# Kernel tuning notes

Hardware: AMD Instinct MI355X
Metric: run time of the kernel (lower is better)

## Reference

```python
import jax, jax.numpy as jnp
import numpy as np

N_EMBD = 1024
EXPAND = 2
D_INNER = N_EMBD * EXPAND          # 2048
D_STATE = 64
N_HEADS = D_INNER // D_STATE       # 32
HEAD_DIM = D_INNER // N_HEADS      # 64
N_GROUPS = 1
D_CONV = 4
N_LAYERS = 48
BATCH, SEQ = 1, 512
PROJ_SIZE = 2 * D_INNER + N_HEADS + 2 * N_GROUPS * D_STATE  # 4256
EPS = 1e-6


def setup_inputs() -> dict:
    key = jax.random.key(0)
    ks = jax.random.split(key, 6)
    init_std = 0.02
    proj_std = 0.02 / np.sqrt(2 * N_LAYERS)
    return {
        "x": jax.random.normal(ks[0], (BATCH, SEQ, N_EMBD), jnp.float32),
        "norm_scale": jnp.ones((N_EMBD,), jnp.float32),
        "w_in": jax.random.normal(ks[1], (N_EMBD, PROJ_SIZE), jnp.float32) * init_std,
        "conv_weight": jax.random.normal(ks[2], (D_CONV, D_INNER), jnp.float32) * 0.02,
        "conv_bias": jnp.zeros((D_INNER,), jnp.float32),
        "A_log": jnp.log(0.5 + jnp.arange(N_HEADS, dtype=jnp.float32) * 0.5 / N_HEADS),
        "dt_bias": jax.random.normal(ks[3], (N_HEADS,), jnp.float32) * 0.1,
        "w_out": jax.random.normal(ks[4], (D_INNER, N_EMBD), jnp.float32) * proj_std,
    }


def _mamba_fwd(x, norm_scale, w_in, conv_weight, conv_bias, A_log, dt_bias, w_out):
    b, T, _ = x.shape
    residual = x
    # RMSNorm
    xn = x * jax.lax.rsqrt(jnp.mean(x * x, axis=-1, keepdims=True) + EPS) * norm_scale
    # in_proj and split
    proj = xn @ w_in  # (b, T, proj_size)
    gate = proj[..., :D_INNER]
    ssm_in = proj[..., D_INNER:2 * D_INNER]
    dt_raw = proj[..., 2 * D_INNER:2 * D_INNER + N_HEADS]
    gs = N_GROUPS * D_STATE
    B = proj[..., 2 * D_INNER + N_HEADS:2 * D_INNER + N_HEADS + gs].reshape(b, T, N_GROUPS, D_STATE)
    C = proj[..., 2 * D_INNER + N_HEADS + gs:].reshape(b, T, N_GROUPS, D_STATE)
    # causal depthwise short conv (cross-correlation, matching lax.conv semantics)
    xp = jnp.pad(ssm_in, ((0, 0), (D_CONV - 1, 0), (0, 0)))
    conv = conv_bias + sum(conv_weight[k] * xp[:, k:k + T, :] for k in range(D_CONV))
    h = jax.nn.silu(conv)  # (b, T, d_inner)
    dt = jax.nn.softplus(dt_raw + dt_bias)  # (b, T, H)
    A = -jnp.exp(A_log)  # (H,)
    A_bar = jnp.exp(A[None, None, :] * dt)  # (b, T, H)
    # heads / groups
    hpg = N_HEADS // N_GROUPS
    xh = h.reshape(b, T, N_HEADS, HEAD_DIM)
    Bh = jnp.repeat(B, hpg, axis=2)  # (b, T, H, N)
    Ch = jnp.repeat(C, hpg, axis=2)  # (b, T, H, N)
    # Bu[b,t,h,p,n] = B[b,t,h,n] * dt[b,t,h] * x[b,t,h,p]
    Bu = Bh[:, :, :, None, :] * (dt[..., None, None] * xh[..., None])  # (b,T,H,P,N)

    def _binary_op(left, right):
        a_l, b_l = left
        a_r, b_r = right
        return (a_l * a_r, a_r * b_l + b_r)

    # A_bar broadcast to (b,T,H,1,1) so the pair broadcasts against Bu
    _, states = jax.lax.associative_scan(_binary_op, (A_bar[..., None, None], Bu), axis=1)
    y = jnp.einsum('bthpn,bthn->bthp', states, Ch).reshape(b, T, D_INNER)
    y = y * jax.nn.silu(gate)
    y = y @ w_out
    return residual + y


def reference(x, norm_scale, w_in, conv_weight, conv_bias, A_log, dt_bias, w_out):
    return _mamba_fwd(x, norm_scale, w_in, conv_weight, conv_bias, A_log, dt_bias, w_out)
```

## Files before the change

### kernel.cpp

```cpp
#include <hip/hip_runtime.h>
#include <hip/hip_bf16.h>

typedef unsigned short u16;
typedef float f32x4v __attribute__((ext_vector_type(4)));
typedef short short8 __attribute__((ext_vector_type(8)));

#define TSEQ 512
#define EMB  1024
#define DI   2048
#define NH   32
#define DS   64
#define PROJ 4256
#define PROJP 4352
#define NCH  8
#define LCH  64
#define KSPLIT2 4

#define MFMA16(a, b, c) __builtin_amdgcn_mfma_f32_16x16x32_bf16(a, b, c, 0, 0, 0)

__device__ __forceinline__ u16 f2bf(float f) {
    union { __hip_bfloat16 h; u16 u; } cv;
    cv.h = __float2bfloat16(f);
    return cv.u;
}
__device__ __forceinline__ unsigned pack2(float a, float b) {
    return (unsigned)f2bf(a) | ((unsigned)f2bf(b) << 16);
}
__device__ __forceinline__ float silu(float v) { return v / (1.f + expf(-v)); }

__device__ __forceinline__ void transpose_tile(
        const float* __restrict__ src, u16* __restrict__ dst,
        int K, int N, int n0, int k0, int tid, float tile[64][68]) {
    const int lr = tid >> 4;
    const int lc = tid & 15;
    #pragma unroll
    for (int ps = 0; ps < 4; ++ps) {
        int r = ps * 16 + lr;
        float4 v;
        if (n0 + lc * 4 + 3 < N) {
            v = *(const float4*)&src[(size_t)(k0 + r) * N + n0 + lc * 4];
        } else {
            float t0 = 0.f, t1 = 0.f, t2 = 0.f, t3 = 0.f;
            int nb = n0 + lc * 4;
            if (nb + 0 < N) t0 = src[(size_t)(k0 + r) * N + nb + 0];
            if (nb + 1 < N) t1 = src[(size_t)(k0 + r) * N + nb + 1];
            if (nb + 2 < N) t2 = src[(size_t)(k0 + r) * N + nb + 2];
            if (nb + 3 < N) t3 = src[(size_t)(k0 + r) * N + nb + 3];
            v = make_float4(t0, t1, t2, t3);
        }
        *(float4*)&tile[r][lc * 4] = v;
    }
    __syncthreads();
    const int kk2 = (tid & 31) * 2;
    const int nr  = tid >> 5;
    #pragma unroll
    for (int ps = 0; ps < 8; ++ps) {
        int n = ps * 8 + nr;
        unsigned o = (unsigned)f2bf(tile[kk2][n]) | ((unsigned)f2bf(tile[kk2 + 1][n]) << 16);
        *(unsigned*)&dst[(size_t)(n0 + n) * K + k0 + kk2] = o;
    }
}

__global__ __launch_bounds__(256) void k_prep(
        const float* __restrict__ w_in, u16* __restrict__ w_inT,
        const float* __restrict__ w_out, u16* __restrict__ w_outT,
        const float* __restrict__ x, const float* __restrict__ scale,
        u16* __restrict__ xnb) {
    __shared__ float tile[64][68];
    const int b = blockIdx.x;
    const int tid = threadIdx.x;
    if (b < 1088) {
        int bx = b % 68, by = b / 68;
        transpose_tile(w_in, w_inT, 1024, PROJ, bx * 64, by * 64, tid, tile);
    } else if (b < 1600) {
        int b2 = b - 1088;
        int bx = b2 % 16, by = b2 / 16;
        transpose_tile(w_out, w_outT, 2048, 1024, bx * 64, by * 64, tid, tile);
    } else {
        int t = b - 1600;
        const float4* xr = (const float4*)(x + (size_t)t * EMB);
        float4 v = xr[tid];
        float ss = v.x * v.x + v.y * v.y + v.z * v.z + v.w * v.w;
        #pragma unroll
        for (int off = 32; off; off >>= 1) ss += __shfl_xor(ss, off);
        if ((tid & 63) == 0) tile[0][tid >> 6] = ss;
        __syncthreads();
        float tot = tile[0][0] + tile[0][1] + tile[0][2] + tile[0][3];
        float inv = rsqrtf(tot * (1.f / EMB) + 1e-6f);
        float4 s = ((const float4*)scale)[tid];
        uint2 o;
        o.x = pack2(v.x * inv * s.x, v.y * inv * s.y);
        o.y = pack2(v.z * inv * s.z, v.w * inv * s.w);
        ((uint2*)xnb)[(size_t)t * 256 + tid] = o;
    }
}

template<int BM, int BN>
__global__ __launch_bounds__(256) void k_gemm(
        const u16* __restrict__ A, int lda,
        const u16* __restrict__ BT, int ldb,
        float* __restrict__ C, int ldc, int Kper) {
    constexpr int WM = BM / 2, WN = BN / 2, FM = WM / 16, FN = WN / 16;
    constexpr int NA = BM * 8 / 256, NB = BN * 8 / 256;
    __shared__ __align__(16) u16 Al[BM][72];
    __shared__ __align__(16) u16 Bl[BN][72];
    const int tid = threadIdx.x;
    const int wid = tid >> 6, lane = tid & 63;
    const int wr = wid >> 1, wc = wid & 1;
    const int ar = lane & 15, kg = lane >> 4;
    const int row0 = blockIdx.y * BM, col0 = blockIdx.x * BN;
    const int kbase = blockIdx.z * Kper;
    const int Mtot = gridDim.y * BM;
    float* Cz = C + (size_t)blockIdx.z * Mtot * ldc;

    short8 ra[NA], rb[NB];
    auto load_stage = [&](int k0) {
        #pragma unroll
        for (int j = 0; j < NA; ++j) {
            int idx = tid + j * 256;
            ra[j] = *(const short8*)(A + (size_t)(row0 + (idx >> 3)) * lda + k0 + (idx & 7) * 8);
        }
        #pragma unroll
        for (int j = 0; j < NB; ++j) {
            int idx = tid + j * 256;
            rb[j] = *(const short8*)(BT + (size_t)(col0 + (idx >> 3)) * ldb + k0 + (idx & 7) * 8);
        }
    };
    auto write_stage = [&]() {
        #pragma unroll
        for (int j = 0; j < NA; ++j) {
            int idx = tid + j * 256;
            *(short8*)&Al[idx >> 3][(idx & 7) * 8] = ra[j];
        }
        #pragma unroll
        for (int j = 0; j < NB; ++j) {
            int idx = tid + j * 256;
            *(short8*)&Bl[idx >> 3][(idx & 7) * 8] = rb[j];
        }
    };

    f32x4v acc[FM][FN] = {};
    const int NT = Kper / 64;
    load_stage(kbase);
    for (int kt = 0; kt < NT; ++kt) {
        write_stage();
        __syncthreads();
        if (kt + 1 < NT) load_stage(kbase + (kt + 1) * 64);
        #pragma unroll
        for (int kk = 0; kk < 2; ++kk) {
            short8 af[FM], bf[FN];
            #pragma unroll
            for (int m = 0; m < FM; ++m)
                af[m] = *(const short8*)&Al[wr * WM + m * 16 + ar][kk * 32 + kg * 8];
            #pragma unroll
            for (int n = 0; n < FN; ++n)
                bf[n] = *(const short8*)&Bl[wc * WN + n * 16 + ar][kk * 32 + kg * 8];
            #pragma unroll
            for (int m = 0; m < FM; ++m)
                #pragma unroll
                for (int n = 0; n < FN; ++n)
                    acc[m][n] = MFMA16(af[m], bf[n], acc[m][n]);
        }
        __syncthreads();
    }
    #pragma unroll
    for (int m = 0; m < FM; ++m)
        #pragma unroll
        for (int n = 0; n < FN; ++n)
            #pragma unroll
            for (int j = 0; j < 4; ++j) {
                int row = row0 + wr * WM + m * 16 + kg * 4 + j;
                int col = col0 + wc * WN + n * 16 + ar;
                Cz[(size_t)row * ldc + col] = acc[m][n][j];
            }
}

__global__ __launch_bounds__(256) void k_reduce_out(
        const float* __restrict__ part, const float* __restrict__ x,
        float* __restrict__ out) {
    int i = blockIdx.x * 256 + threadIdx.x;
    float4 v = ((const float4*)x)[i];
    #pragma unroll
    for (int z = 0; z < KSPLIT2; ++z) {
        float4 p = ((const float4*)part)[(size_t)z * (TSEQ * EMB / 4) + i];
        v.x += p.x; v.y += p.y; v.z += p.z; v.w += p.w;
    }
    ((float4*)out)[i] = v;
}

__global__ __launch_bounds__(256) void k_ssd(
        const float* __restrict__ proj, const float* __restrict__ cw,
        const float* __restrict__ cb, const float* __restrict__ A_log,
        const float* __restrict__ dt_bias,
        float* __restrict__ Sloc, float* __restrict__ Lacum,
        float* __restrict__ yloc) {
    const int c = blockIdx.x, h = blockIdx.y;
    const int tid = threadIdx.x;
    const int w = tid >> 6, lane = tid & 63;
    const int ar = lane & 15, kg = lane >> 4;
    __shared__ __align__(16) u16 Bl[64][72];
    __shared__ __align__(16) u16 BlTw[64][72];
    __shared__ __align__(16) u16 Cl[64][72];
    __shared__ __align__(16) u16 XlT[64][72];
    __shared__ __align__(16) u16 Gl[64][72];
    __shared__ float xt[67][68];
    __shared__ float la[64], dl[64];
    for (int i = tid; i < 67 * 64; i += 256) {
        int r = i >> 6, n = i & 63;
        int tt = c * 64 - 3 + r;
        xt[r][n] = (tt >= 0) ? proj[(size_t)tt * PROJP + DI + h * 64 + n] : 0.f;
    }
    if (tid < 64) {
        float z = proj[(size_t)(c * 64 + tid) * PROJP + 2 * DI + h] + dt_bias[h];
        dl[tid] = (z > 20.f) ? z : log1pf(expf(z));
    }
    __syncthreads();
    if (tid < 64) {
        float cum = 0.f;
        #pragma unroll
        for (int k = 0; k < 64; ++k) if (k <= tid) cum += dl[k];
        float lav = -expf(A_log[h]) * cum;
        la[tid] = lav;
        Lacum[((size_t)(c * 32 + h)) * 64 + tid] = lav;
    }
    __syncthreads();
    const float la63 = la[63];
    for (int i = tid; i < 4096; i += 256) {
        int t = i >> 6, n = i & 63;
        size_t rowoff = (size_t)(c * 64 + t) * PROJP + 2 * DI + NH;
        float bv = proj[rowoff + n];
        float cv = proj[rowoff + DS + n];
        Bl[t][n] = f2bf(bv);
        Cl[t][n] = f2bf(cv);
        BlTw[n][t] = f2bf(bv * expf(la63 - la[t]));
        int ch = h * 64 + n;
        float conv = cb[ch]
                   + cw[0 * DI + ch] * xt[t][n]     + cw[1 * DI + ch] * xt[t + 1][n]
                   + cw[2 * DI + ch] * xt[t + 2][n] + cw[3 * DI + ch] * xt[t + 3][n];
        XlT[n][t] = f2bf(dl[t] * silu(conv));
    }
    __syncthreads();
    f32x4v accG[4] = {};
    #pragma unroll
    for (int kk = 0; kk < 2; ++kk) {
        short8 af = *(const short8*)&Cl[w * 16 + ar][kk * 32 + kg * 8];
        #pragma unroll
        for (int tc = 0; tc < 4; ++tc) {
            short8 bf = *(const short8*)&Bl[tc * 16 + ar][kk * 32 + kg * 8];
            accG[tc] = MFMA16(af, bf, accG[tc]);
        }
    }
    #pragma unroll
    for (int tc = 0; tc < 4; ++tc) {
        int tp = tc * 16 + ar;
        #pragma unroll
        for (int j = 0; j < 4; ++j) {
            int t = w * 16 + kg * 4 + j;
            float v = (tp <= t) ? accG[tc][j] * expf(la[t] - la[tp]) : 0.f;
            Gl[t][tp] = f2bf(v);
        }
    }
    __syncthreads();
    f32x4v accY[4] = {}, accS[4] = {};
    #pragma unroll
    for (int kk = 0; kk < 2; ++kk) {
        short8 ag = *(const short8*)&Gl[w * 16 + ar][kk * 32 + kg * 8];
        short8 ab = *(const short8*)&BlTw[w * 16 + ar][kk * 32 + kg * 8];
        #pragma unroll
        for (int tc = 0; tc < 4; ++tc) {
            short8 bx = *(const short8*)&XlT[tc * 16 + ar][kk * 32 + kg * 8];
            accY[tc] = MFMA16(ag, bx, accY[tc]);
            accS[tc] = MFMA16(ab, bx, accS[tc]);
        }
    }
    float* slc = Sloc + ((size_t)(c * 32 + h)) * 4096;
    #pragma unroll
    for (int tc = 0; tc < 4; ++tc) {
        int p = tc * 16 + ar;
        #pragma unroll
        for (int j = 0; j < 4; ++j) {
            int r = w * 16 + kg * 4 + j;
            yloc[(size_t)(c * 64 + r) * DI + h * 64 + p] = accY[tc][j];
            slc[p * 64 + r] = accS[tc][j];
        }
    }
}

__global__ __launch_bounds__(256) void k_scan2(
        const float* __restrict__ Sloc, const float* __restrict__ Lacum,
        float* __restrict__ Sinit) {
    int gid = blockIdx.x * 256 + threadIdx.x;
    int h = gid >> 12, rem = gid & 4095;
    float s = 0.f;
    #pragma unroll
    for (int cc = 0; cc < NCH; ++cc) {
        size_t o = (size_t)(cc * 32 + h) * 4096 + rem;
        Sinit[o] = s;
        float ptot = expf(Lacum[((size_t)(cc * 32 + h)) * 64 + 63]);
        s = ptot * s + Sloc[o];
    }
}

__global__ __launch_bounds__(256) void k_corr2(
        const float* __restrict__ proj, const float* __restrict__ Sinit,
        const float* __restrict__ Lacum, const float* __restrict__ yloc,
        u16* __restrict__ yg) {
    const int c = blockIdx.x, h = blockIdx.y;
    const int tid = threadIdx.x;
    const int w = tid >> 6, lane = tid & 63;
    const int ar = lane & 15, kg = lane >> 4;
    __shared__ __align__(16) u16 Cl[64][72];
    __shared__ __align__(16) u16 Sl[64][72];
    __shared__ float la[64];
    const float* sic = Sinit + ((size_t)(c * 32 + h)) * 4096;
    for (int i = tid; i < 4096; i += 256) {
        int t = i >> 6, n = i & 63;
        Cl[t][n] = f2bf(proj[(size_t)(c * 64 + t) * PROJP + 2 * DI + NH + DS + n]);
        Sl[t][n] = f2bf(sic[i]);
    }
    if (tid < 64) la[tid] = Lacum[((size_t)(c * 32 + h)) * 64 + tid];
    __syncthreads();
    f32x4v acc[4] = {};
    #pragma unroll
    for (int kk = 0; kk < 2; ++kk) {
        short8 ac = *(const short8*)&Cl[w * 16 + ar][kk * 32 + kg * 8];
        #pragma unroll
        for (int tc = 0; tc < 4; ++tc) {
            short8 bs = *(const short8*)&Sl[tc * 16 + ar][kk * 32 + kg * 8];
            acc[tc] = MFMA16(ac, bs, acc[tc]);
        }
    }
    #pragma unroll
    for (int tc = 0; tc < 4; ++tc) {
        int p = tc * 16 + ar;
        #pragma unroll
        for (int j = 0; j < 4; ++j) {
            int t = w * 16 + kg * 4 + j;
            float y = yloc[(size_t)(c * 64 + t) * DI + h * 64 + p]
                    + expf(la[t]) * acc[tc][j];
            float g = proj[(size_t)(c * 64 + t) * PROJP + h * 64 + p];
            yg[(size_t)(c * 64 + t) * DI + h * 64 + p] = f2bf(y * silu(g));
        }
    }
}

extern "C" void kernel_launch(void* const* d_in, const int* in_sizes, int n_in,
                              void* d_out, int out_size, void* d_ws, size_t ws_size,
                              hipStream_t stream) {
    (void)in_sizes; (void)n_in; (void)out_size; (void)ws_size;
    const float* x       = (const float*)d_in[0];
    const float* nscale  = (const float*)d_in[1];
    const float* w_in    = (const float*)d_in[2];
    const float* conv_w  = (const float*)d_in[3];
    const float* conv_b  = (const float*)d_in[4];
    const float* A_log   = (const float*)d_in[5];
    const float* dt_bias = (const float*)d_in[6];
    const float* w_out   = (const float*)d_in[7];
    float* out = (float*)d_out;

    char* wsp = (char*)d_ws;
    auto alloc = [&](size_t bytes) {
        char* ptr = wsp;
        wsp += (bytes + 255) & ~(size_t)255;
        return ptr;
    };
    u16*   w_inT  = (u16*)  alloc((size_t)PROJP * 1024 * 2);
    u16*   w_outT = (u16*)  alloc((size_t)1024 * 2048 * 2);
    u16*   xnb    = (u16*)  alloc((size_t)512 * 1024 * 2);
    float* proj   = (float*)alloc((size_t)512 * PROJP * 4);
    float* Lacum  = (float*)alloc((size_t)NCH * 32 * 64 * 4);
    float* Sloc   = (float*)alloc((size_t)NCH * 32 * 4096 * 4);
    float* Sinit  = (float*)alloc((size_t)NCH * 32 * 4096 * 4);
    float* yloc   = (float*)alloc((size_t)512 * 2048 * 4);
    u16*   yg     = (u16*)  alloc((size_t)512 * 2048 * 2);
    float* part2  = (float*)alloc((size_t)KSPLIT2 * 512 * 1024 * 4);

    k_prep<<<2112, 256, 0, stream>>>(w_in, w_inT, w_out, w_outT, x, nscale, xnb);
    k_gemm<32, 128><<<dim3(34, 16, 1), 256, 0, stream>>>(
        xnb, 1024, w_inT, 1024, proj, PROJP, 1024);
    k_ssd<<<dim3(NCH, 32), 256, 0, stream>>>(
        proj, conv_w, conv_b, A_log, dt_bias, Sloc, Lacum, yloc);
    k_scan2<<<512, 256, 0, stream>>>(Sloc, Lacum, Sinit);
    k_corr2<<<dim3(NCH, 32), 256, 0, stream>>>(proj, Sinit, Lacum, yloc, yg);
    k_gemm<32, 128><<<dim3(8, 16, KSPLIT2), 256, 0, stream>>>(
        yg, 2048, w_outT, 2048, part2, 1024, 2048 / KSPLIT2);
    k_reduce_out<<<512, 256, 0, stream>>>(part2, x, out);
}
```

Measured before the change: 143.9 us.

## Fuse inter-chunk state scan into correction kernel and widen GEMM K tile

Removes the separate k_scan2 kernel and its Sinit buffer. Each k_corr2 block now recomputes its chunk's initial state by accumulating the earlier chunks' local states from Sloc, weighted by their decay factors. This saves a launch and a full global write and read of the states, at the cost of redundant sequential work for later chunks. The GEMM template also gains a BK parameter set to 128, halving the number of K iterations and barriers at the cost of more LDS and registers per block.

```diff
diff --git a/kernel.cpp b/kernel.cpp
--- a/kernel.cpp
+++ b/kernel.cpp
@@ -95,15 +95,16 @@
     }
 }
 
-template<int BM, int BN>
+template<int BM, int BN, int BK>
 __global__ __launch_bounds__(256) void k_gemm(
         const u16* __restrict__ A, int lda,
         const u16* __restrict__ BT, int ldb,
         float* __restrict__ C, int ldc, int Kper) {
     constexpr int WM = BM / 2, WN = BN / 2, FM = WM / 16, FN = WN / 16;
-    constexpr int NA = BM * 8 / 256, NB = BN * 8 / 256;
-    __shared__ __align__(16) u16 Al[BM][72];
-    __shared__ __align__(16) u16 Bl[BN][72];
+    constexpr int CPR = BK / 8;
+    constexpr int NA = BM * CPR / 256, NB = BN * CPR / 256;
+    __shared__ __align__(16) u16 Al[BM][BK + 8];
+    __shared__ __align__(16) u16 Bl[BN][BK + 8];
     const int tid = threadIdx.x;
     const int wid = tid >> 6, lane = tid & 63;
     const int wr = wid >> 1, wc = wid & 1;
@@ -118,36 +119,36 @@
         #pragma unroll
         for (int j = 0; j < NA; ++j) {
             int idx = tid + j * 256;
-            ra[j] = *(const short8*)(A + (size_t)(row0 + (idx >> 3)) * lda + k0 + (idx & 7) * 8);
+            ra[j] = *(const short8*)(A + (size_t)(row0 + idx / CPR) * lda + k0 + (idx % CPR) * 8);
         }
         #pragma unroll
         for (int j = 0; j < NB; ++j) {
             int idx = tid + j * 256;
-            rb[j] = *(const short8*)(BT + (size_t)(col0 + (idx >> 3)) * ldb + k0 + (idx & 7) * 8);
+            rb[j] = *(const short8*)(BT + (size_t)(col0 + idx / CPR) * ldb + k0 + (idx % CPR) * 8);
         }
     };
     auto write_stage = [&]() {
         #pragma unroll
         for (int j = 0; j < NA; ++j) {
             int idx = tid + j * 256;
-            *(short8*)&Al[idx >> 3][(idx & 7) * 8] = ra[j];
+            *(short8*)&Al[idx / CPR][(idx % CPR) * 8] = ra[j];
         }
         #pragma unroll
         for (int j = 0; j < NB; ++j) {
             int idx = tid + j * 256;
-            *(short8*)&Bl[idx >> 3][(idx & 7) * 8] = rb[j];
+            *(short8*)&Bl[idx / CPR][(idx % CPR) * 8] = rb[j];
         }
     };
 
     f32x4v acc[FM][FN] = {};
-    const int NT = Kper / 64;
+    const int NT = Kper / BK;
     load_stage(kbase);
     for (int kt = 0; kt < NT; ++kt) {
         write_stage();
         __syncthreads();
-        if (kt + 1 < NT) load_stage(kbase + (kt + 1) * 64);
-        #pragma unroll
-        for (int kk = 0; kk < 2; ++kk) {
+        if (kt + 1 < NT) load_stage(kbase + (kt + 1) * BK);
+        #pragma unroll
+        for (int kk = 0; kk < BK / 32; ++kk) {
             short8 af[FM], bf[FN];
             #pragma unroll
             for (int m = 0; m < FM; ++m)
@@ -286,23 +287,8 @@
     }
 }
 
-__global__ __launch_bounds__(256) void k_scan2(
-        const float* __restrict__ Sloc, const float* __restrict__ Lacum,
-        float* __restrict__ Sinit) {
-    int gid = blockIdx.x * 256 + threadIdx.x;
-    int h = gid >> 12, rem = gid & 4095;
-    float s = 0.f;
-    #pragma unroll
-    for (int cc = 0; cc < NCH; ++cc) {
-        size_t o = (size_t)(cc * 32 + h) * 4096 + rem;
-        Sinit[o] = s;
-        float ptot = expf(Lacum[((size_t)(cc * 32 + h)) * 64 + 63]);
-        s = ptot * s + Sloc[o];
-    }
-}
-
 __global__ __launch_bounds__(256) void k_corr2(
-        const float* __restrict__ proj, const float* __restrict__ Sinit,
+        const float* __restrict__ proj, const float* __restrict__ Sloc,
         const float* __restrict__ Lacum, const float* __restrict__ yloc,
         u16* __restrict__ yg) {
     const int c = blockIdx.x, h = blockIdx.y;
@@ -312,13 +298,29 @@
     __shared__ __align__(16) u16 Cl[64][72];
     __shared__ __align__(16) u16 Sl[64][72];
     __shared__ float la[64];
-    const float* sic = Sinit + ((size_t)(c * 32 + h)) * 4096;
+    __shared__ float ptl[NCH];
     for (int i = tid; i < 4096; i += 256) {
         int t = i >> 6, n = i & 63;
         Cl[t][n] = f2bf(proj[(size_t)(c * 64 + t) * PROJP + 2 * DI + NH + DS + n]);
-        Sl[t][n] = f2bf(sic[i]);
     }
     if (tid < 64) la[tid] = Lacum[((size_t)(c * 32 + h)) * 64 + tid];
+    if (tid >= 64 && tid < 64 + NCH)
+        ptl[tid - 64] = expf(Lacum[((size_t)((tid - 64) * 32 + h)) * 64 + 63]);
+    __syncthreads();
+    #pragma unroll
+    for (int i4 = 0; i4 < 4; ++i4) {
+        int rem = i4 * 1024 + tid * 4;
+        float4 s = make_float4(0.f, 0.f, 0.f, 0.f);
+        for (int cc = 0; cc < c; ++cc) {
+            float pt = ptl[cc];
+            float4 v = *(const float4*)&Sloc[((size_t)(cc * 32 + h)) * 4096 + rem];
+            s.x = pt * s.x + v.x; s.y = pt * s.y + v.y;
+            s.z = pt * s.z + v.z; s.w = pt * s.w + v.w;
+        }
+        int p = rem >> 6, n = rem & 63;
+        *(unsigned*)&Sl[p][n]     = pack2(s.x, s.y);
+        *(unsigned*)&Sl[p][n + 2] = pack2(s.z, s.w);
+    }
     __syncthreads();
     f32x4v acc[4] = {};
     #pragma unroll
@@ -370,19 +372,17 @@
     float* proj   = (float*)alloc((size_t)512 * PROJP * 4);
     float* Lacum  = (float*)alloc((size_t)NCH * 32 * 64 * 4);
     float* Sloc   = (float*)alloc((size_t)NCH * 32 * 4096 * 4);
-    float* Sinit  = (float*)alloc((size_t)NCH * 32 * 4096 * 4);
     float* yloc   = (float*)alloc((size_t)512 * 2048 * 4);
     u16*   yg     = (u16*)  alloc((size_t)512 * 2048 * 2);
     float* part2  = (float*)alloc((size_t)KSPLIT2 * 512 * 1024 * 4);
 
     k_prep<<<2112, 256, 0, stream>>>(w_in, w_inT, w_out, w_outT, x, nscale, xnb);
-    k_gemm<32, 128><<<dim3(34, 16, 1), 256, 0, stream>>>(
+    k_gemm<32, 128, 128><<<dim3(34, 16, 1), 256, 0, stream>>>(
         xnb, 1024, w_inT, 1024, proj, PROJP, 1024);
     k_ssd<<<dim3(NCH, 32), 256, 0, stream>>>(
         proj, conv_w, conv_b, A_log, dt_bias, Sloc, Lacum, yloc);
-    k_scan2<<<512, 256, 0, stream>>>(Sloc, Lacum, Sinit);
-    k_corr2<<<dim3(NCH, 32), 256, 0, stream>>>(proj, Sinit, Lacum, yloc, yg);
-    k_gemm<32, 128><<<dim3(8, 16, KSPLIT2), 256, 0, stream>>>(
+    k_corr2<<<dim3(NCH, 32), 256, 0, stream>>>(proj, Sloc, Lacum, yloc, yg);
+    k_gemm<32, 128, 128><<<dim3(8, 16, KSPLIT2), 256, 0, stream>>>(
         yg, 2048, w_outT, 2048, part2, 1024, 2048 / KSPLIT2);
     k_reduce_out<<<512, 256, 0, stream>>>(part2, x, out);
 }
```

New measurement: 145.4 us. Within noise of the previous version (+1.0%).
